# Performance work log

Hardware: AMD Instinct MI355X
Metric: run time of the kernel (lower is better)

The kernel has to match this reference:

```python
import jax, jax.numpy as jnp
import numpy as np

MARGIN = 0.8
EPS = 1e-6  # torch F.pairwise_distance eps added to the difference


def setup_inputs() -> dict:
    key = jax.random.key(0)
    k1, k2, k3 = jax.random.split(key, 3)
    B, D = 8192, 128
    emb = jax.random.normal(k1, (B, D), dtype=jnp.float32)
    labels = jax.random.randint(k2, (B,), 0, 6)
    sbj = jax.random.randint(k3, (B,), 0, 16)
    return {"emb": emb, "labels": labels, "sbj": sbj}


def reference(emb, labels, sbj):
    B = emb.shape[0]
    # Squared pairwise distances (monotone in true distance -> same argmax/argmin)
    sq = jnp.sum(emb * emb, axis=1)
    d2 = sq[:, None] + sq[None, :] - 2.0 * (emb @ emb.T)  # [B, B]
    same_s = sbj[:, None] == sbj[None, :]
    same_l = labels[:, None] == labels[None, :]
    eye = jnp.eye(B, dtype=bool)
    pos_m = same_s & same_l & ~eye          # within-subject, same label, not self
    neg_m = same_s & ~same_l                # within-subject, different label
    valid = pos_m.any(axis=1) & neg_m.any(axis=1)
    p_idx = jnp.argmax(jnp.where(pos_m, d2, -jnp.inf), axis=1)  # hardest positive
    n_idx = jnp.argmin(jnp.where(neg_m, d2, jnp.inf), axis=1)   # hardest negative
    # TripletMarginLoss(p=2): pairwise_distance adds eps to the difference
    dap = jnp.linalg.norm(emb - emb[p_idx] + EPS, axis=1)
    dan = jnp.linalg.norm(emb - emb[n_idx] + EPS, axis=1)
    per = jnp.maximum(dap - dan + MARGIN, 0.0)
    cnt = jnp.sum(valid)
    loss = jnp.sum(jnp.where(valid, per, 0.0)) / jnp.maximum(cnt, 1)
    return jnp.where(cnt > 0, loss, 0.0)
```

## Files before the change

kernel.cpp:

```cpp
#include <hip/hip_runtime.h>
#include <math.h>
#include <limits.h>

#define D 128
#define NSUBJ 16
#define MAXN 640
#define MARGIN 0.8f
#define PRB 32
#define NPB 256
#define TI 16
#define TJ 64
#define NSTRIPE 32
#define NBLK (NSUBJ * NSTRIPE)

typedef __attribute__((ext_vector_type(8))) short bf16x8;
typedef __attribute__((ext_vector_type(4))) float f32x4;

static __device__ __forceinline__ short f2bf(float f) {
    union { float f; unsigned u; } v; v.f = f;
    unsigned r = v.u + 0x7FFF + ((v.u >> 16) & 1);
    return (short)(r >> 16);
}

static __device__ __forceinline__ void gload_lds16(const void* g, void* l) {
    __builtin_amdgcn_global_load_lds(
        (const __attribute__((address_space(1))) void*)g,
        (__attribute__((address_space(3))) void*)l, 16, 0, 0);
}

__global__ __launch_bounds__(64) void hist_kernel(const int* __restrict__ sbj,
                                                  int* __restrict__ hist) {
    __shared__ int s_cnt[NSUBJ];
    const int t = threadIdx.x, bid = blockIdx.x;
    if (t < NSUBJ) s_cnt[t] = 0;
    __syncthreads();
    if (t < PRB) atomicAdd(&s_cnt[sbj[bid * PRB + t]], 1);
    __syncthreads();
    if (t < NSUBJ) hist[bid * NSUBJ + t] = s_cnt[t];
}

__global__ __launch_bounds__(256) void prep_kernel(
        const float* __restrict__ emb, const int* __restrict__ labels,
        const int* __restrict__ sbj, const int* __restrict__ hist,
        int* __restrict__ counts,
        int4* __restrict__ pmeta, short* __restrict__ ebf, int B) {
    __shared__ int s_cnt[NSUBJ], s_base[NSUBJ], s_slot[PRB];
    const int t = threadIdx.x, bid = blockIdx.x;
    if (t < NSUBJ) { s_cnt[t] = 0; s_base[t] = 0; }
    __syncthreads();
    {
        const int ss = t & 15, seg0 = (t >> 4) * 16;
        int part = 0;
        const int hi = min(bid, seg0 + 16);
        for (int b = seg0; b < hi; ++b) part += hist[b * NSUBJ + ss];
        if (part) atomicAdd(&s_base[ss], part);
    }
    int s = 0, mypos = 0;
    if (t < PRB) { s = sbj[bid * PRB + t]; mypos = atomicAdd(&s_cnt[s], 1); }
    __syncthreads();
    if (t < PRB) {
        int pos = s_base[s] + mypos;
        s_slot[t] = (pos < MAXN) ? (s * MAXN + pos) : -1;
    }
    if (bid == NPB - 1 && t < NSUBJ)
        counts[t] = s_base[t] + s_cnt[t];
    __syncthreads();
#pragma unroll
    for (int it = 0; it < (PRB * 16) / 256; ++it) {
        int lin = it * 256 + t;
        int row = lin >> 4, u = lin & 15;
        int i = bid * PRB + row;
        int slot = s_slot[row];
        const float4* rp = (const float4*)(emb + (size_t)i * D);
        float4 a0 = rp[u * 2], a1 = rp[u * 2 + 1];
        float ssq = 0.f;
        ssq = fmaf(a0.x, a0.x, ssq); ssq = fmaf(a0.y, a0.y, ssq);
        ssq = fmaf(a0.z, a0.z, ssq); ssq = fmaf(a0.w, a0.w, ssq);
        ssq = fmaf(a1.x, a1.x, ssq); ssq = fmaf(a1.y, a1.y, ssq);
        ssq = fmaf(a1.z, a1.z, ssq); ssq = fmaf(a1.w, a1.w, ssq);
#pragma unroll
        for (int off = 8; off > 0; off >>= 1) ssq += __shfl_down(ssq, off, 16);
        if (slot >= 0) {
            bf16x8 pk;
            pk[0] = f2bf(a0.x); pk[1] = f2bf(a0.y); pk[2] = f2bf(a0.z); pk[3] = f2bf(a0.w);
            pk[4] = f2bf(a1.x); pk[5] = f2bf(a1.y); pk[6] = f2bf(a1.z); pk[7] = f2bf(a1.w);
            *(bf16x8*)&ebf[(size_t)slot * D + u * 8] = pk;
            if (u == 0)
                pmeta[slot] = make_int4(labels[i], i, __float_as_int(ssq), 0);
        }
    }
}

#define STAGE(BUF, JT)                                                    \
    do {                                                                  \
        const char* ts_ = (const char*)ebf + ((size_t)(base + (JT) * TJ)) * 256; \
        _Pragma("unroll")                                                 \
        for (int ii_ = 0; ii_ < 4; ++ii_) {                               \
            int lin_ = ((w * 4 + ii_) * 64 + lane) * 16;                  \
            int row_ = lin_ >> 8;                                         \
            gload_lds16(ts_ + (lin_ ^ ((row_ & 7) << 4)),                 \
                        ldsB + (BUF) * (TJ * 256) + (w * 4 + ii_) * 1024);\
        }                                                                 \
    } while (0)

__global__ __launch_bounds__(256, 2) void triplet_kernel(
        const short* __restrict__ ebf, const int4* __restrict__ pmeta,
        const int* __restrict__ counts,
        float* __restrict__ bsum, int* __restrict__ bcnt) {
    const int bid = blockIdx.x, t = threadIdx.x;
    const int s = bid & 15;
    const int stripe = bid >> 4;
    const int base = s * MAXN;
    const int n = min(counts[s], MAXN);
    const int lane = t & 63, w = t >> 6, c = lane & 15, q = lane >> 4;

    __shared__ char ldsB[2 * TJ * 256];
    __shared__ char ldsM[MAXN * 16];
    __shared__ float svP[TI][4]; __shared__ int siP[TI][4];
    __shared__ float svN[TI][4]; __shared__ int siN[TI][4];

    const int ntiles = (n + TJ - 1) / TJ;

    for (int r = w; r < ntiles; r += 4)
        gload_lds16((const char*)(pmeta + base + r * 64) + lane * 16,
                    ldsM + r * 1024);

    float blockSum = 0.f; int blockCnt = 0;

    for (int i0 = stripe * TI; i0 < n; i0 += NSTRIPE * TI) {
        const int nrows = min(TI, n - i0);

        bf16x8 afr[4];
        {
            const short* ap = ebf + (size_t)(base + i0 + min(c, nrows - 1)) * D;
#pragma unroll
            for (int st = 0; st < 4; ++st)
                afr[st] = *(const bf16x8*)&ap[st * 32 + q * 8];
        }
        int li[4], gI[4];
#pragma unroll
        for (int r = 0; r < 4; ++r) {
            int row = q * 4 + r;
            if (row < nrows) { int4 m = pmeta[base + i0 + row]; li[r] = m.x; gI[r] = m.y; }
            else             { li[r] = INT_MIN; gI[r] = -1; }
        }

        float vP[4], vN[4]; int iP[4], iN[4];
#pragma unroll
        for (int r = 0; r < 4; ++r) {
            vP[r] = -INFINITY; iP[r] = -1;
            vN[r] =  INFINITY; iN[r] = -1;
        }

        STAGE(0, 0);
        if (1 < ntiles) STAGE(1, 1);
        int cur = 0;

        for (int jt = 0; jt < ntiles; ++jt) {
            if (jt + 1 < ntiles) asm volatile("s_waitcnt vmcnt(4)" ::: "memory");
            else                 asm volatile("s_waitcnt vmcnt(0)" ::: "memory");
            __builtin_amdgcn_sched_barrier(0);
            __builtin_amdgcn_s_barrier();
            __builtin_amdgcn_sched_barrier(0);

            {
                const char* bb = ldsB + cur * (TJ * 256);
                const int lr = w * 16 + c, swz = (lr & 7) << 4;
                bf16x8 f0 = *(const bf16x8*)(bb + lr * 256 + ((  0 + q * 16) ^ swz));
                bf16x8 f1 = *(const bf16x8*)(bb + lr * 256 + (( 64 + q * 16) ^ swz));
                bf16x8 f2 = *(const bf16x8*)(bb + lr * 256 + ((128 + q * 16) ^ swz));
                bf16x8 f3 = *(const bf16x8*)(bb + lr * 256 + ((192 + q * 16) ^ swz));
                const int jl = jt * TJ + lr;
                int4 m = *(const int4*)(ldsM + jl * 16);
                const int MI = (jl < n) ? m.y : -1;
                const int ML = m.x; const float MS = __int_as_float(m.z);

                f32x4 acc = {0.f, 0.f, 0.f, 0.f};
                acc = __builtin_amdgcn_mfma_f32_16x16x32_bf16(afr[0], f0, acc, 0, 0, 0);
                acc = __builtin_amdgcn_mfma_f32_16x16x32_bf16(afr[1], f1, acc, 0, 0, 0);
                acc = __builtin_amdgcn_mfma_f32_16x16x32_bf16(afr[2], f2, acc, 0, 0, 0);
                acc = __builtin_amdgcn_mfma_f32_16x16x32_bf16(afr[3], f3, acc, 0, 0, 0);
                if (MI >= 0) {
#pragma unroll
                    for (int r = 0; r < 4; ++r) {
                        float v = fmaf(-2.f, acc[r], MS);
                        if (ML == li[r]) {
                            if (MI != gI[r] && v > vP[r]) { vP[r] = v; iP[r] = MI; }
                        } else if (v < vN[r]) { vN[r] = v; iN[r] = MI; }
                    }
                }
            }

            __builtin_amdgcn_s_barrier();
            __builtin_amdgcn_sched_barrier(0);
            if (jt + 2 < ntiles) STAGE(cur, jt + 2);
            cur ^= 1;
        }

#pragma unroll
        for (int off = 8; off > 0; off >>= 1) {
#pragma unroll
            for (int r = 0; r < 4; ++r) {
                float ov = __shfl_down(vP[r], off, 16);
                int   oi = __shfl_down(iP[r], off, 16);
                if (ov > vP[r] || (ov == vP[r] && (unsigned)oi < (unsigned)iP[r])) {
                    vP[r] = ov; iP[r] = oi;
                }
                float on = __shfl_down(vN[r], off, 16);
                int   oj = __shfl_down(iN[r], off, 16);
                if (on < vN[r] || (on == vN[r] && (unsigned)oj < (unsigned)iN[r])) {
                    vN[r] = on; iN[r] = oj;
                }
            }
        }
        if (c == 0) {
#pragma unroll
            for (int r = 0; r < 4; ++r) {
                int row = q * 4 + r;
                svP[row][w] = vP[r]; siP[row][w] = iP[r];
                svN[row][w] = vN[r]; siN[row][w] = iN[r];
            }
        }
        __syncthreads();

        if (t < TI) {
            float bp = svP[t][0]; int ip = siP[t][0];
            float bn = svN[t][0]; int in_ = siN[t][0];
#pragma unroll
            for (int ww = 1; ww < 4; ++ww) {
                float o = svP[t][ww]; int oi = siP[t][ww];
                if (o > bp || (o == bp && (unsigned)oi < (unsigned)ip)) { bp = o; ip = oi; }
                float on = svN[t][ww]; int oj = siN[t][ww];
                if (on < bn || (on == bn && (unsigned)oj < (unsigned)in_)) { bn = on; in_ = oj; }
            }
            bool valid = (t < nrows) && (ip >= 0) && (in_ >= 0);
            float sqi = __int_as_float(
                ((const int4*)(ldsM + (i0 + min(t, nrows - 1)) * 16))->z);
            float per = 0.f;
            if (valid) {
                float dap = sqrtf(fmaxf(bp + sqi, 0.f));
                float dan = sqrtf(fmaxf(bn + sqi, 0.f));
                per = fmaxf(dap - dan + MARGIN, 0.f);
            }
            int vc = valid ? 1 : 0;
#pragma unroll
            for (int off = 8; off > 0; off >>= 1) {
                per += __shfl_down(per, off, 16);
                vc  += __shfl_down(vc,  off, 16);
            }
            if (t == 0) { blockSum += per; blockCnt += vc; }
        }
        if (i0 + NSTRIPE * TI < n) __syncthreads();
    }

    if (t == 0) { bsum[bid] = blockSum; bcnt[bid] = blockCnt; }
}

__global__ __launch_bounds__(256) void finalize_kernel(
        const float* __restrict__ bsum, const int* __restrict__ bcnt,
        float* __restrict__ out) {
    __shared__ float ssum[4]; __shared__ int scnt[4];
    const int t = threadIdx.x;
    float s = 0.f; int c = 0;
#pragma unroll
    for (int i = t; i < NBLK; i += 256) { s += bsum[i]; c += bcnt[i]; }
#pragma unroll
    for (int off = 32; off > 0; off >>= 1) {
        s += __shfl_down(s, off, 64);
        c += __shfl_down(c, off, 64);
    }
    if ((t & 63) == 0) { ssum[t >> 6] = s; scnt[t >> 6] = c; }
    __syncthreads();
    if (t == 0) {
        float S = ssum[0] + ssum[1] + ssum[2] + ssum[3];
        int   C = scnt[0] + scnt[1] + scnt[2] + scnt[3];
        out[0] = (C > 0) ? (S / (float)C) : 0.0f;
    }
}

extern "C" void kernel_launch(void* const* d_in, const int* in_sizes, int n_in,
                              void* d_out, int out_size, void* d_ws, size_t ws_size,
                              hipStream_t stream) {
    const float* emb    = (const float*)d_in[0];
    const int*   labels = (const int*)d_in[1];
    const int*   sbj    = (const int*)d_in[2];
    float*       out    = (float*)d_out;
    int B = in_sizes[1];

    char*  ws        = (char*)d_ws;
    int*   counts    = (int*)ws;
    float* bsum      = (float*)(ws + 256);
    int*   bcnt      = (int*)(ws + 256 + NBLK * sizeof(float));
    int*   hist      = (int*)(ws + 256 + 2 * NBLK * sizeof(int));
    size_t pmeta_off = (256 + 2 * (size_t)NBLK * sizeof(int)
                        + (size_t)NPB * NSUBJ * sizeof(int) + 255) & ~(size_t)255;
    int4*  pmeta     = (int4*)(ws + pmeta_off);
    size_t ebf_off   = (pmeta_off + (size_t)NSUBJ * MAXN * sizeof(int4) + 255) & ~(size_t)255;
    short* ebf       = (short*)(ws + ebf_off);

    hist_kernel<<<B / PRB, 64, 0, stream>>>(sbj, hist);
    prep_kernel<<<B / PRB, 256, 0, stream>>>(emb, labels, sbj, hist, counts,
                                             pmeta, ebf, B);
    triplet_kernel<<<NBLK, 256, 0, stream>>>(ebf, pmeta, counts, bsum, bcnt);
    finalize_kernel<<<1, 256, 0, stream>>>(bsum, bcnt, out);
}
```

Baseline: 86.27 us.

## Process two 16-row query tiles per block to reuse staged column tiles

Each block now handles 32 query rows as two MFMA row tiles that share every staged 64-column B tile in LDS. The stripe count is halved, so half as many blocks run and B-tile loads per row drop by half. The cost is more registers per thread (launch bounds minimum occupancy lowered to 1) and fewer blocks overall (256), which may leave parts of the GPU underused and hurt latency hiding.

```diff
diff --git a/kernel.cpp b/kernel.cpp
--- a/kernel.cpp
+++ b/kernel.cpp
@@ -9,8 +9,9 @@
 #define PRB 32
 #define NPB 256
 #define TI 16
+#define TIB 32
 #define TJ 64
-#define NSTRIPE 32
+#define NSTRIPE 16
 #define NBLK (NSUBJ * NSTRIPE)
 
 typedef __attribute__((ext_vector_type(8))) short bf16x8;
@@ -103,7 +104,18 @@
         }                                                                 \
     } while (0)
 
-__global__ __launch_bounds__(256, 2) void triplet_kernel(
+#define SELECT(ACC, LI, GI, VP, IP, VN, IN, MI, ML, MS)                   \
+    do {                                                                  \
+        _Pragma("unroll")                                                 \
+        for (int r = 0; r < 4; ++r) {                                     \
+            float v = fmaf(-2.f, (ACC)[r], (MS));                         \
+            if ((ML) == (LI)[r]) {                                        \
+                if ((MI) != (GI)[r] && v > (VP)[r]) { (VP)[r] = v; (IP)[r] = (MI); } \
+            } else if (v < (VN)[r]) { (VN)[r] = v; (IN)[r] = (MI); }      \
+        }                                                                 \
+    } while (0)
+
+__global__ __launch_bounds__(256, 1) void triplet_kernel(
         const short* __restrict__ ebf, const int4* __restrict__ pmeta,
         const int* __restrict__ counts,
         float* __restrict__ bsum, int* __restrict__ bcnt) {
@@ -116,8 +128,8 @@
 
     __shared__ char ldsB[2 * TJ * 256];
     __shared__ char ldsM[MAXN * 16];
-    __shared__ float svP[TI][4]; __shared__ int siP[TI][4];
-    __shared__ float svN[TI][4]; __shared__ int siN[TI][4];
+    __shared__ float svP[TIB][4]; __shared__ int siP[TIB][4];
+    __shared__ float svN[TIB][4]; __shared__ int siN[TIB][4];
 
     const int ntiles = (n + TJ - 1) / TJ;
 
@@ -127,29 +139,38 @@
 
     float blockSum = 0.f; int blockCnt = 0;
 
-    for (int i0 = stripe * TI; i0 < n; i0 += NSTRIPE * TI) {
-        const int nrows = min(TI, n - i0);
-
-        bf16x8 afr[4];
+    for (int i0 = stripe * TIB; i0 < n; i0 += NSTRIPE * TIB) {
+        const int nrows = min(TIB, n - i0);
+        const int nr0 = min(nrows, TI);
+        const int nr1 = nrows - nr0;
+
+        bf16x8 afr0[4], afr1[4];
         {
-            const short* ap = ebf + (size_t)(base + i0 + min(c, nrows - 1)) * D;
-#pragma unroll
-            for (int st = 0; st < 4; ++st)
-                afr[st] = *(const bf16x8*)&ap[st * 32 + q * 8];
-        }
-        int li[4], gI[4];
+            const short* ap0 = ebf + (size_t)(base + i0 + min(c, nr0 - 1)) * D;
+            const int r1 = (nr1 > 0) ? (i0 + TI + min(c, nr1 - 1)) : i0;
+            const short* ap1 = ebf + (size_t)(base + r1) * D;
+#pragma unroll
+            for (int st = 0; st < 4; ++st) {
+                afr0[st] = *(const bf16x8*)&ap0[st * 32 + q * 8];
+                afr1[st] = *(const bf16x8*)&ap1[st * 32 + q * 8];
+            }
+        }
+        int li0[4], gI0[4], li1[4], gI1[4];
 #pragma unroll
         for (int r = 0; r < 4; ++r) {
             int row = q * 4 + r;
-            if (row < nrows) { int4 m = pmeta[base + i0 + row]; li[r] = m.x; gI[r] = m.y; }
-            else             { li[r] = INT_MIN; gI[r] = -1; }
-        }
-
-        float vP[4], vN[4]; int iP[4], iN[4];
+            if (row < nr0) { int4 m = pmeta[base + i0 + row];      li0[r] = m.x; gI0[r] = m.y; }
+            else           { li0[r] = INT_MIN; gI0[r] = -1; }
+            if (row < nr1) { int4 m = pmeta[base + i0 + TI + row]; li1[r] = m.x; gI1[r] = m.y; }
+            else           { li1[r] = INT_MIN; gI1[r] = -1; }
+        }
+
+        float vP0[4], vN0[4], vP1[4], vN1[4];
+        int   iP0[4], iN0[4], iP1[4], iN1[4];
 #pragma unroll
         for (int r = 0; r < 4; ++r) {
-            vP[r] = -INFINITY; iP[r] = -1;
-            vN[r] =  INFINITY; iN[r] = -1;
+            vP0[r] = -INFINITY; iP0[r] = -1; vN0[r] = INFINITY; iN0[r] = -1;
+            vP1[r] = -INFINITY; iP1[r] = -1; vN1[r] = INFINITY; iN1[r] = -1;
         }
 
         STAGE(0, 0);
@@ -175,19 +196,19 @@
                 const int MI = (jl < n) ? m.y : -1;
                 const int ML = m.x; const float MS = __int_as_float(m.z);
 
-                f32x4 acc = {0.f, 0.f, 0.f, 0.f};
-                acc = __builtin_amdgcn_mfma_f32_16x16x32_bf16(afr[0], f0, acc, 0, 0, 0);
-                acc = __builtin_amdgcn_mfma_f32_16x16x32_bf16(afr[1], f1, acc, 0, 0, 0);
-                acc = __builtin_amdgcn_mfma_f32_16x16x32_bf16(afr[2], f2, acc, 0, 0, 0);
-                acc = __builtin_amdgcn_mfma_f32_16x16x32_bf16(afr[3], f3, acc, 0, 0, 0);
+                f32x4 acc0 = {0.f, 0.f, 0.f, 0.f};
+                acc0 = __builtin_amdgcn_mfma_f32_16x16x32_bf16(afr0[0], f0, acc0, 0, 0, 0);
+                acc0 = __builtin_amdgcn_mfma_f32_16x16x32_bf16(afr0[1], f1, acc0, 0, 0, 0);
+                acc0 = __builtin_amdgcn_mfma_f32_16x16x32_bf16(afr0[2], f2, acc0, 0, 0, 0);
+                acc0 = __builtin_amdgcn_mfma_f32_16x16x32_bf16(afr0[3], f3, acc0, 0, 0, 0);
+                f32x4 acc1 = {0.f, 0.f, 0.f, 0.f};
+                acc1 = __builtin_amdgcn_mfma_f32_16x16x32_bf16(afr1[0], f0, acc1, 0, 0, 0);
+                acc1 = __builtin_amdgcn_mfma_f32_16x16x32_bf16(afr1[1], f1, acc1, 0, 0, 0);
+                acc1 = __builtin_amdgcn_mfma_f32_16x16x32_bf16(afr1[2], f2, acc1, 0, 0, 0);
+                acc1 = __builtin_amdgcn_mfma_f32_16x16x32_bf16(afr1[3], f3, acc1, 0, 0, 0);
                 if (MI >= 0) {
-#pragma unroll
-                    for (int r = 0; r < 4; ++r) {
-                        float v = fmaf(-2.f, acc[r], MS);
-                        if (ML == li[r]) {
-                            if (MI != gI[r] && v > vP[r]) { vP[r] = v; iP[r] = MI; }
-                        } else if (v < vN[r]) { vN[r] = v; iN[r] = MI; }
-                    }
+                    SELECT(acc0, li0, gI0, vP0, iP0, vN0, iN0, MI, ML, MS);
+                    SELECT(acc1, li1, gI1, vP1, iP1, vN1, iN1, MI, ML, MS);
                 }
             }
 
@@ -201,29 +222,30 @@
         for (int off = 8; off > 0; off >>= 1) {
 #pragma unroll
             for (int r = 0; r < 4; ++r) {
-                float ov = __shfl_down(vP[r], off, 16);
-                int   oi = __shfl_down(iP[r], off, 16);
-                if (ov > vP[r] || (ov == vP[r] && (unsigned)oi < (unsigned)iP[r])) {
-                    vP[r] = ov; iP[r] = oi;
-                }
-                float on = __shfl_down(vN[r], off, 16);
-                int   oj = __shfl_down(iN[r], off, 16);
-                if (on < vN[r] || (on == vN[r] && (unsigned)oj < (unsigned)iN[r])) {
-                    vN[r] = on; iN[r] = oj;
-                }
+                float ov; int oi;
+                ov = __shfl_down(vP0[r], off, 16); oi = __shfl_down(iP0[r], off, 16);
+                if (ov > vP0[r] || (ov == vP0[r] && (unsigned)oi < (unsigned)iP0[r])) { vP0[r] = ov; iP0[r] = oi; }
+                ov = __shfl_down(vN0[r], off, 16); oi = __shfl_down(iN0[r], off, 16);
+                if (ov < vN0[r] || (ov == vN0[r] && (unsigned)oi < (unsigned)iN0[r])) { vN0[r] = ov; iN0[r] = oi; }
+                ov = __shfl_down(vP1[r], off, 16); oi = __shfl_down(iP1[r], off, 16);
+                if (ov > vP1[r] || (ov == vP1[r] && (unsigned)oi < (unsigned)iP1[r])) { vP1[r] = ov; iP1[r] = oi; }
+                ov = __shfl_down(vN1[r], off, 16); oi = __shfl_down(iN1[r], off, 16);
+                if (ov < vN1[r] || (ov == vN1[r] && (unsigned)oi < (unsigned)iN1[r])) { vN1[r] = ov; iN1[r] = oi; }
             }
         }
         if (c == 0) {
 #pragma unroll
             for (int r = 0; r < 4; ++r) {
                 int row = q * 4 + r;
-                svP[row][w] = vP[r]; siP[row][w] = iP[r];
-                svN[row][w] = vN[r]; siN[row][w] = iN[r];
+                svP[row][w] = vP0[r]; siP[row][w] = iP0[r];
+                svN[row][w] = vN0[r]; siN[row][w] = iN0[r];
+                svP[TI + row][w] = vP1[r]; siP[TI + row][w] = iP1[r];
+                svN[TI + row][w] = vN1[r]; siN[TI + row][w] = iN1[r];
             }
         }
         __syncthreads();
 
-        if (t < TI) {
+        if (t < TIB) {
             float bp = svP[t][0]; int ip = siP[t][0];
             float bn = svN[t][0]; int in_ = siN[t][0];
 #pragma unroll
@@ -244,13 +266,13 @@
             }
             int vc = valid ? 1 : 0;
 #pragma unroll
-            for (int off = 8; off > 0; off >>= 1) {
-                per += __shfl_down(per, off, 16);
-                vc  += __shfl_down(vc,  off, 16);
+            for (int off = 16; off > 0; off >>= 1) {
+                per += __shfl_down(per, off, 32);
+                vc  += __shfl_down(vc,  off, 32);
             }
             if (t == 0) { blockSum += per; blockCnt += vc; }
         }
-        if (i0 + NSTRIPE * TI < n) __syncthreads();
+        if (i0 + NSTRIPE * TIB < n) __syncthreads();
     }
 
     if (t == 0) { bsum[bid] = blockSum; bcnt[bid] = blockCnt; }
```

Result: slower. 98.41 us (+14.1%).
